# Optimization experiments

Hardware: AMD Instinct MI355X
Metric: run time of the kernel (lower is better)

Reference implementation:

```python
import jax, jax.numpy as jnp
import numpy as np

B, C, H, W = 1, 512, 24, 24
N_HEADS, WS = 8, 7
PAD = WS // 2
HEAD_DIM = C // N_HEADS


def setup_inputs() -> dict:
    key = jax.random.key(0)
    ks = jax.random.split(key, 7)
    s = 0.02
    return {
        "x": jax.random.normal(ks[0], (B, C, H, W), dtype=jnp.float32),
        "Wq": s * jax.random.normal(ks[1], (C, C), dtype=jnp.float32),
        "bq": s * jax.random.normal(ks[2], (C,), dtype=jnp.float32),
        "Wk": s * jax.random.normal(ks[3], (C, C), dtype=jnp.float32),
        "bk": s * jax.random.normal(ks[4], (C,), dtype=jnp.float32),
        "Wv": s * jax.random.normal(ks[5], (C, C), dtype=jnp.float32),
        "bv": s * jax.random.normal(ks[6], (C,), dtype=jnp.float32),
        # module initializes gamma to zero; use small nonzero so output depends on attention
        "gamma": jnp.full((1,), 0.1, dtype=jnp.float32),
    }


def _conv1x1(z, Wt, bt):
    # 1x1 Conv2d == per-pixel GEMM over channels
    return jnp.einsum("bchw,oc->bohw", z, Wt) + bt[None, :, None, None]


def _windows(z):
    # z: (B, C, H+ws-1, W+ws-1) -> (B, n_heads, head_dim, ws*ws*H*W)
    # matches torch unfold(2,ws,1).unfold(3,ws,1).permute(0,1,4,5,2,3).view(...)
    taps = [z[:, :, di:di + H, dj:dj + W] for di in range(WS) for dj in range(WS)]
    w = jnp.stack(taps, axis=2)  # (B, C, ws*ws, H, W)
    return w.reshape(B, N_HEADS, HEAD_DIM, WS * WS * H * W)


def reference(x, Wq, bq, Wk, bk, Wv, bv, gamma):
    q = _conv1x1(x, Wq, bq).reshape(B, N_HEADS, HEAD_DIM, H * W)  # (B,h,d,HW)
    xp = jnp.pad(x, ((0, 0), (0, 0), (PAD, PAD), (PAD, PAD)), mode="reflect")
    k = _windows(_conv1x1(xp, Wk, bk))  # (B,h,d,ws^2*HW)
    v = _windows(_conv1x1(xp, Wv, bv))  # (B,h,d,ws^2*HW)
    # NOTE: as written in the source, each query attends to ALL ws^2*H*W keys
    energy = jnp.einsum("bhdq,bhdk->bhqk", q, k)  # (B,h,HW,ws^2*HW)
    attn = jax.nn.softmax(energy, axis=-1)
    out_w = jnp.einsum("bhqk,bhdk->bhdq", attn, v).reshape(B, C, H, W)
    return gamma * out_w + x
```

## Files before the change

### kernel.cpp

```cpp
#include <hip/hip_runtime.h>

#define HW   576
#define CC   512
#define PW   30
#define PPK  1024

typedef float f32x4 __attribute__((ext_vector_type(4)));
typedef short s16x8 __attribute__((ext_vector_type(8)));

__device__ __forceinline__ unsigned short f2bf(float f) {
    unsigned u = __float_as_uint(f);
    return (unsigned short)((u + 0x7FFFu + ((u >> 16) & 1u)) >> 16);
}
__device__ __forceinline__ float bf2f(unsigned short h) {
    return __uint_as_float((unsigned)h << 16);
}
__device__ __forceinline__ int smapf(int p) {
    if (p >= 900) return 576;
    const int y = p / PW, xw = p - y * PW;
    int iy = y - 3;  iy = (iy < 0) ? -iy : (iy > 23 ? 46 - iy : iy);
    int ix = xw - 3; ix = (ix < 0) ? -ix : (ix > 23 ? 46 - ix : ix);
    return iy * 24 + ix;
}

#define OFF_QT 0u
#define OFF_KT 589824u
#define OFF_VP 1638400u
#define OFF_XT 2686976u
#define OFF_WB 3277824u

__global__ __launch_bounds__(256) void cvtT(
    const float* __restrict__ x,
    const float* __restrict__ Wq, const float* __restrict__ Wk,
    const float* __restrict__ Wv,
    unsigned short* __restrict__ xT, unsigned short* __restrict__ wb)
{
    const int b = blockIdx.x, t = threadIdx.x;
    if (b < 72) {
        __shared__ float tile[64][65];
        const int pt = b % 9, ct = b / 9;
        const int p0 = pt * 64, c0 = ct * 64;
        const int tr = t >> 4, tc4 = (t & 15) * 4;
        #pragma unroll
        for (int cr = 0; cr < 4; ++cr) {
            const int row = cr * 16 + tr;
            const float4 v = *(const float4*)&x[(size_t)(c0 + row) * HW + p0 + tc4];
            tile[row][tc4 + 0] = v.x;
            tile[row][tc4 + 1] = v.y;
            tile[row][tc4 + 2] = v.z;
            tile[row][tc4 + 3] = v.w;
        }
        __syncthreads();
        #pragma unroll
        for (int cr = 0; cr < 4; ++cr) {
            const int prow = cr * 16 + tr;
            ushort4 o;
            o.x = f2bf(tile[tc4 + 0][prow]);
            o.y = f2bf(tile[tc4 + 1][prow]);
            o.z = f2bf(tile[tc4 + 2][prow]);
            o.w = f2bf(tile[tc4 + 3][prow]);
            *(ushort4*)&xT[(size_t)(p0 + prow) * CC + c0 + tc4] = o;
        }
    } else if (b == 72) {
        if (t < 128) *(ushort4*)&xT[(size_t)576 * CC + t * 4] = (ushort4){0, 0, 0, 0};
    } else {
        const int wi = (b - 73) * 2048 + t * 8;
        const int sel = wi >> 18, off = wi & 262143;
        const float* src = (sel == 0) ? Wq : (sel == 1) ? Wk : Wv;
        const float4 v0 = *(const float4*)&src[off];
        const float4 v1 = *(const float4*)&src[off + 4];
        ushort4 o0, o1;
        o0.x = f2bf(v0.x); o0.y = f2bf(v0.y); o0.z = f2bf(v0.z); o0.w = f2bf(v0.w);
        o1.x = f2bf(v1.x); o1.y = f2bf(v1.y); o1.z = f2bf(v1.z); o1.w = f2bf(v1.w);
        *(ushort4*)&wb[wi]     = o0;
        *(ushort4*)&wb[wi + 4] = o1;
    }
}

__global__ __launch_bounds__(256) void qkv_direct(
    const unsigned short* __restrict__ xT, const unsigned short* __restrict__ wb,
    const float* __restrict__ bq, const float* __restrict__ bk,
    const float* __restrict__ bv,
    unsigned short* __restrict__ qT, unsigned short* __restrict__ kT,
    unsigned short* __restrict__ vP)
{
    const int t = threadIdx.x;
    const int w = blockIdx.x * 4 + (t >> 6);
    const int lane = t & 63, fr = lane & 15, u = lane >> 4;

    int sel, m0, n0;
    if (w < 288)      { sel = 0; m0 = (w >> 4) << 5;               n0 = (w & 15) << 5; }
    else if (w < 800) { const int k = w - 288; sel = 1; m0 = (k >> 4) << 5; n0 = (k & 15) << 5; }
    else              { const int k = w - 800; sel = 2; m0 = (k >> 5) << 5; n0 = (k & 31) << 5; }

    const unsigned short *A, *B;
    int ar0, ar1, bn0, bn1;
    if (sel == 0)      { A = xT;          B = wb;
                         ar0 = m0 + fr;         ar1 = m0 + 16 + fr;
                         bn0 = n0 + fr;         bn1 = n0 + 16 + fr; }
    else if (sel == 1) { A = xT;          B = wb + 262144;
                         ar0 = smapf(m0 + fr);  ar1 = smapf(m0 + 16 + fr);
                         bn0 = n0 + fr;         bn1 = n0 + 16 + fr; }
    else               { A = wb + 524288; B = xT;
                         ar0 = m0 + fr;         ar1 = m0 + 16 + fr;
                         bn0 = smapf(n0 + fr);  bn1 = smapf(n0 + 16 + fr); }

    const unsigned short* Ap0 = A + (size_t)ar0 * CC + u * 8;
    const unsigned short* Ap1 = A + (size_t)ar1 * CC + u * 8;
    const unsigned short* Bp0 = B + (size_t)bn0 * CC + u * 8;
    const unsigned short* Bp1 = B + (size_t)bn1 * CC + u * 8;

    f32x4 acc00 = (f32x4){0.f, 0.f, 0.f, 0.f};
    f32x4 acc01 = (f32x4){0.f, 0.f, 0.f, 0.f};
    f32x4 acc10 = (f32x4){0.f, 0.f, 0.f, 0.f};
    f32x4 acc11 = (f32x4){0.f, 0.f, 0.f, 0.f};
    #pragma unroll 4
    for (int k0 = 0; k0 < CC; k0 += 32) {
        const s16x8 a0 = *(const s16x8*)(Ap0 + k0);
        const s16x8 a1 = *(const s16x8*)(Ap1 + k0);
        const s16x8 b0 = *(const s16x8*)(Bp0 + k0);
        const s16x8 b1 = *(const s16x8*)(Bp1 + k0);
        acc00 = __builtin_amdgcn_mfma_f32_16x16x32_bf16(a0, b0, acc00, 0, 0, 0);
        acc01 = __builtin_amdgcn_mfma_f32_16x16x32_bf16(a0, b1, acc01, 0, 0, 0);
        acc10 = __builtin_amdgcn_mfma_f32_16x16x32_bf16(a1, b0, acc10, 0, 0, 0);
        acc11 = __builtin_amdgcn_mfma_f32_16x16x32_bf16(a1, b1, acc11, 0, 0, 0);
    }

    #pragma unroll
    for (int mi = 0; mi < 2; ++mi) {
        #pragma unroll
        for (int ni = 0; ni < 2; ++ni) {
            const f32x4 acc = mi ? (ni ? acc11 : acc10) : (ni ? acc01 : acc00);
            const int n = n0 + ni * 16 + fr;
            #pragma unroll
            for (int r = 0; r < 4; ++r) {
                const int m = m0 + mi * 16 + u * 4 + r;
                if (sel == 0) {
                    qT[((size_t)(n >> 6) * HW + m) * 64 + (n & 63)] = f2bf(acc[r] + bq[n]);
                } else if (sel == 1) {
                    kT[((size_t)(n >> 6) * PPK + m) * 64 + (n & 63)] = f2bf(acc[r] + bk[n]);
                } else {
                    vP[((size_t)(m >> 6) * 64 + (m & 63)) * PPK + n] = f2bf(acc[r] + bv[m]);
                }
            }
        }
    }
}

#define WLS 1040
__global__ __launch_bounds__(512) void attn5(
    const unsigned short* __restrict__ qT, const unsigned short* __restrict__ kT,
    const unsigned short* __restrict__ vP, const float* __restrict__ x,
    const float* __restrict__ gamma, float* __restrict__ out)
{
    const int q0 = blockIdx.x * 16;
    const int hd = blockIdx.y;
    const int t  = threadIdx.x;
    const int lane = t & 63, w = t >> 6;
    const int fr = lane & 15, u = lane >> 4;

    __shared__ float cnt_s[PPK];
    __shared__ __align__(16) unsigned short Wl[16 * WLS];
    __shared__ float mw[128], lw[128], sca[16];
    __shared__ float4 red[4][64];

    for (int i = t; i < PPK; i += 512) {
        float c = 0.f;
        if (i < 900) {
            const int y = i / PW, xw = i - y * PW;
            int cy = y + 1;  if (PW - y  < cy) cy = PW - y;  if (cy > 7) cy = 7;
            int cx = xw + 1; if (PW - xw < cx) cx = PW - xw; if (cx > 7) cx = 7;
            c = (float)(cy * cx);
        }
        cnt_s[i] = c;
    }

    const unsigned short* qrow = qT + ((size_t)hd * HW + q0 + fr) * 64 + u * 8;
    const s16x8 b0 = *(const s16x8*)qrow;
    const s16x8 b1 = *(const s16x8*)(qrow + 32);

    f32x4 e[8];
    #pragma unroll
    for (int t4 = 0; t4 < 8; ++t4) {
        const unsigned short* krow =
            kT + ((size_t)hd * PPK + w * 128 + t4 * 16 + fr) * 64 + u * 8;
        const s16x8 a0 = *(const s16x8*)krow;
        const s16x8 a1 = *(const s16x8*)(krow + 32);
        f32x4 a = (f32x4){0.f, 0.f, 0.f, 0.f};
        a = __builtin_amdgcn_mfma_f32_16x16x32_bf16(a0, b0, a, 0, 0, 0);
        a = __builtin_amdgcn_mfma_f32_16x16x32_bf16(a1, b1, a, 0, 0, 0);
        e[t4] = a;
    }

    float m = -1e30f;
    #pragma unroll
    for (int t4 = 0; t4 < 8; ++t4)
        #pragma unroll
        for (int r = 0; r < 4; ++r) m = fmaxf(m, e[t4][r]);
    m = fmaxf(m, __shfl_xor(m, 16));
    m = fmaxf(m, __shfl_xor(m, 32));
    if (lane < 16) mw[w * 16 + lane] = m;
    __syncthreads();
    float mq = mw[fr];
    #pragma unroll
    for (int j = 1; j < 8; ++j) mq = fmaxf(mq, mw[j * 16 + fr]);

    float sum = 0.f;
    #pragma unroll
    for (int t4 = 0; t4 < 8; ++t4) {
        const float4 c4 = *(const float4*)&cnt_s[w * 128 + t4 * 16 + u * 4];
        const float cw[4] = {c4.x, c4.y, c4.z, c4.w};
        unsigned short wb4[4];
        #pragma unroll
        for (int r = 0; r < 4; ++r) {
            const float wv2 = cw[r] * __expf(e[t4][r] - mq);
            sum += wv2;
            wb4[r] = f2bf(wv2);
        }
        const int ho = fr * WLS + w * 128 + t4 * 16 + u * 4;
        *(unsigned*)&Wl[ho]     = (unsigned)wb4[0] | ((unsigned)wb4[1] << 16);
        *(unsigned*)&Wl[ho + 2] = (unsigned)wb4[2] | ((unsigned)wb4[3] << 16);
    }
    sum += __shfl_xor(sum, 16);
    sum += __shfl_xor(sum, 32);
    if (lane < 16) lw[w * 16 + lane] = sum;
    __syncthreads();

    if (t < 16) {
        float lq = 0.f;
        #pragma unroll
        for (int j = 0; j < 8; ++j) lq += lw[j * 16 + t];
        sca[t] = gamma[0] / lq;
    }

    const int dt = w & 3, ph = w >> 2;
    f32x4 o = (f32x4){0.f, 0.f, 0.f, 0.f};
    const unsigned short* vrow =
        vP + ((size_t)hd * 64 + dt * 16 + fr) * PPK + ph * 512 + u * 8;
    #pragma unroll 8
    for (int c = 0; c < 16; ++c) {
        const s16x8 aw = *(const s16x8*)&Wl[fr * WLS + ph * 512 + c * 32 + u * 8];
        const s16x8 bv2 = *(const s16x8*)(vrow + c * 32);
        o = __builtin_amdgcn_mfma_f32_16x16x32_bf16(aw, bv2, o, 0, 0, 0);
    }
    if (w >= 4) red[dt][lane] = (float4){o[0], o[1], o[2], o[3]};
    __syncthreads();
    if (w >= 4) return;

    const float4 r2 = red[dt][lane];
    const int d = hd * 64 + dt * 16 + fr;
    const size_t gb = (size_t)d * HW + q0 + u * 4;
    const float4 x4 = *(const float4*)&x[gb];
    float4 o4;
    o4.x = fmaf(sca[u * 4 + 0], o[0] + r2.x, x4.x);
    o4.y = fmaf(sca[u * 4 + 1], o[1] + r2.y, x4.y);
    o4.z = fmaf(sca[u * 4 + 2], o[2] + r2.z, x4.z);
    o4.w = fmaf(sca[u * 4 + 3], o[3] + r2.w, x4.w);
    *(float4*)&out[gb] = o4;
}

extern "C" void kernel_launch(void* const* d_in, const int* in_sizes, int n_in,
                              void* d_out, int out_size, void* d_ws, size_t ws_size,
                              hipStream_t stream) {
    const float* x     = (const float*)d_in[0];
    const float* Wq    = (const float*)d_in[1];
    const float* bq    = (const float*)d_in[2];
    const float* Wk    = (const float*)d_in[3];
    const float* bk    = (const float*)d_in[4];
    const float* Wv    = (const float*)d_in[5];
    const float* bv    = (const float*)d_in[6];
    const float* gamma = (const float*)d_in[7];
    float* out = (float*)d_out;

    char* wsb = (char*)d_ws;
    unsigned short* qT = (unsigned short*)(wsb + OFF_QT);
    unsigned short* kT = (unsigned short*)(wsb + OFF_KT);
    unsigned short* vP = (unsigned short*)(wsb + OFF_VP);
    unsigned short* xT = (unsigned short*)(wsb + OFF_XT);
    unsigned short* wb = (unsigned short*)(wsb + OFF_WB);

    cvtT<<<dim3(457), 256, 0, stream>>>(x, Wq, Wk, Wv, xT, wb);
    qkv_direct<<<dim3(328), 256, 0, stream>>>(xT, wb, bq, bk, bv, qT, kT, vP);
    attn5<<<dim3(36, 8), 512, 0, stream>>>(qT, kT, vP, x, gamma, out);
}
```

Measured before the change: 107.7 us.

## Split QKV GEMM reduction dimension across four waves with LDS reduction

The QKV projection kernel now gives each 32x32 output tile a whole block of four waves instead of one wave. Each wave accumulates a quarter of the K dimension, and the partial sums are then reduced through shared memory. This raises the number of waves from 1312 spread over 328 blocks to 1312 blocks, which should improve occupancy and shorten each wave's serial MFMA chain. The cost is an LDS round trip, a block barrier and more blocks to launch.

```diff
diff --git a/kernel.cpp b/kernel.cpp
--- a/kernel.cpp
+++ b/kernel.cpp
@@ -77,21 +77,22 @@
     }
 }
 
-__global__ __launch_bounds__(256) void qkv_direct(
+__global__ __launch_bounds__(256) void qkv_ks(
     const unsigned short* __restrict__ xT, const unsigned short* __restrict__ wb,
     const float* __restrict__ bq, const float* __restrict__ bk,
     const float* __restrict__ bv,
     unsigned short* __restrict__ qT, unsigned short* __restrict__ kT,
     unsigned short* __restrict__ vP)
 {
+    const int b = blockIdx.x;
     const int t = threadIdx.x;
-    const int w = blockIdx.x * 4 + (t >> 6);
-    const int lane = t & 63, fr = lane & 15, u = lane >> 4;
+    const int lane = t & 63, w = t >> 6;
+    const int fr = lane & 15, u = lane >> 4;
 
     int sel, m0, n0;
-    if (w < 288)      { sel = 0; m0 = (w >> 4) << 5;               n0 = (w & 15) << 5; }
-    else if (w < 800) { const int k = w - 288; sel = 1; m0 = (k >> 4) << 5; n0 = (k & 15) << 5; }
-    else              { const int k = w - 800; sel = 2; m0 = (k >> 5) << 5; n0 = (k & 31) << 5; }
+    if (b < 288)      { sel = 0; m0 = (b >> 4) << 5;               n0 = (b & 15) << 5; }
+    else if (b < 800) { const int k = b - 288; sel = 1; m0 = (k >> 4) << 5; n0 = (k & 15) << 5; }
+    else              { const int k = b - 800; sel = 2; m0 = (k >> 5) << 5; n0 = (k & 31) << 5; }
 
     const unsigned short *A, *B;
     int ar0, ar1, bn0, bn1;
@@ -105,17 +106,18 @@
                          ar0 = m0 + fr;         ar1 = m0 + 16 + fr;
                          bn0 = smapf(n0 + fr);  bn1 = smapf(n0 + 16 + fr); }
 
-    const unsigned short* Ap0 = A + (size_t)ar0 * CC + u * 8;
-    const unsigned short* Ap1 = A + (size_t)ar1 * CC + u * 8;
-    const unsigned short* Bp0 = B + (size_t)bn0 * CC + u * 8;
-    const unsigned short* Bp1 = B + (size_t)bn1 * CC + u * 8;
+    const int kw = w * 128;
+    const unsigned short* Ap0 = A + (size_t)ar0 * CC + kw + u * 8;
+    const unsigned short* Ap1 = A + (size_t)ar1 * CC + kw + u * 8;
+    const unsigned short* Bp0 = B + (size_t)bn0 * CC + kw + u * 8;
+    const unsigned short* Bp1 = B + (size_t)bn1 * CC + kw + u * 8;
 
     f32x4 acc00 = (f32x4){0.f, 0.f, 0.f, 0.f};
     f32x4 acc01 = (f32x4){0.f, 0.f, 0.f, 0.f};
     f32x4 acc10 = (f32x4){0.f, 0.f, 0.f, 0.f};
     f32x4 acc11 = (f32x4){0.f, 0.f, 0.f, 0.f};
-    #pragma unroll 4
-    for (int k0 = 0; k0 < CC; k0 += 32) {
+    #pragma unroll
+    for (int k0 = 0; k0 < 128; k0 += 32) {
         const s16x8 a0 = *(const s16x8*)(Ap0 + k0);
         const s16x8 a1 = *(const s16x8*)(Ap1 + k0);
         const s16x8 b0 = *(const s16x8*)(Bp0 + k0);
@@ -126,23 +128,28 @@
         acc11 = __builtin_amdgcn_mfma_f32_16x16x32_bf16(a1, b1, acc11, 0, 0, 0);
     }
 
-    #pragma unroll
-    for (int mi = 0; mi < 2; ++mi) {
-        #pragma unroll
-        for (int ni = 0; ni < 2; ++ni) {
-            const f32x4 acc = mi ? (ni ? acc11 : acc10) : (ni ? acc01 : acc00);
-            const int n = n0 + ni * 16 + fr;
-            #pragma unroll
-            for (int r = 0; r < 4; ++r) {
-                const int m = m0 + mi * 16 + u * 4 + r;
-                if (sel == 0) {
-                    qT[((size_t)(n >> 6) * HW + m) * 64 + (n & 63)] = f2bf(acc[r] + bq[n]);
-                } else if (sel == 1) {
-                    kT[((size_t)(n >> 6) * PPK + m) * 64 + (n & 63)] = f2bf(acc[r] + bk[n]);
-                } else {
-                    vP[((size_t)(m >> 6) * 64 + (m & 63)) * PPK + n] = f2bf(acc[r] + bv[m]);
-                }
-            }
+    __shared__ __align__(16) f32x4 red[4][4][64];
+    red[w][0][lane] = acc00;
+    red[w][1][lane] = acc01;
+    red[w][2][lane] = acc10;
+    red[w][3][lane] = acc11;
+    __syncthreads();
+
+    f32x4 v = red[0][w][lane];
+    #pragma unroll
+    for (int w2 = 1; w2 < 4; ++w2) v = v + red[w2][w][lane];
+
+    const int mi = w >> 1, ni = w & 1;
+    const int n = n0 + ni * 16 + fr;
+    #pragma unroll
+    for (int r = 0; r < 4; ++r) {
+        const int m = m0 + mi * 16 + u * 4 + r;
+        if (sel == 0) {
+            qT[((size_t)(n >> 6) * HW + m) * 64 + (n & 63)] = f2bf(v[r] + bq[n]);
+        } else if (sel == 1) {
+            kT[((size_t)(n >> 6) * PPK + m) * 64 + (n & 63)] = f2bf(v[r] + bk[n]);
+        } else {
+            vP[((size_t)(m >> 6) * 64 + (m & 63)) * PPK + n] = f2bf(v[r] + bv[m]);
         }
     }
 }
@@ -280,6 +287,6 @@
     unsigned short* wb = (unsigned short*)(wsb + OFF_WB);
 
     cvtT<<<dim3(457), 256, 0, stream>>>(x, Wq, Wk, Wv, xT, wb);
-    qkv_direct<<<dim3(328), 256, 0, stream>>>(xT, wb, bq, bk, bv, qT, kT, vP);
+    qkv_ks<<<dim3(1312), 256, 0, stream>>>(xT, wb, bq, bk, bv, qT, kT, vP);
     attn5<<<dim3(36, 8), 512, 0, stream>>>(qT, kT, vP, x, gamma, out);
 }
```

Result: faster. 103.6 us (-3.8%).
